# Performance work log

Measured on AMD Instinct MI355X. Metric: run time of the kernel, lower is better.

## Reference

```python
import jax, jax.numpy as jnp
import numpy as np

E_REF = 2.0e11
I_REF = 1.0e-6
Q_REF = 1.0e3
L = 1.0
N = 262144
H = 64


def setup_inputs() -> dict:
    key = jax.random.key(0)
    ks = jax.random.split(key, 8)
    x = jax.random.uniform(ks[0], (N, 1), dtype=jnp.float32) * L
    E = (0.5 + jax.random.uniform(ks[1], (N, 1), dtype=jnp.float32)) * E_REF
    I = (0.5 + jax.random.uniform(ks[2], (N, 1), dtype=jnp.float32)) * I_REF
    q = (0.5 + jax.random.uniform(ks[3], (N, 1), dtype=jnp.float32)) * Q_REF

    def xavier(k, fin, fout):
        std = np.sqrt(2.0 / (fin + fout)).astype(np.float32)
        return jax.random.normal(k, (fin, fout), dtype=jnp.float32) * std

    return dict(
        x=x, E=E, I=I, q=q,
        W1=xavier(ks[4], 4, H), b1=jnp.zeros((H,), jnp.float32),
        W2=xavier(ks[5], H, H), b2=jnp.zeros((H,), jnp.float32),
        W3=xavier(ks[6], H, H), b3=jnp.zeros((H,), jnp.float32),
        W4=xavier(ks[7], H, 1), b4=jnp.zeros((1,), jnp.float32),
    )


def reference(x, E, I, q, W1, b1, W2, b2, W3, b3, W4, b4):
    # per-point scalar network psi(x; E, I, q)
    def psi_scalar(xs, feats):  # xs: scalar, feats: [3] = (E/E_ref, I/I_ref, q/q_ref)
        inp = jnp.concatenate([xs[None], feats])  # [4]
        h = jnp.tanh(inp @ W1 + b1)
        h = jnp.tanh(h @ W2 + b2)
        h = jnp.tanh(h @ W3 + b3)
        return (h @ W4 + b4)[0]

    d1 = jax.grad(psi_scalar)
    d2 = jax.grad(d1)
    d3 = jax.grad(d2)
    d4 = jax.grad(d3)

    feats = jnp.concatenate([E / E_REF, I / I_REF, q / Q_REF], axis=1)  # [N,3]
    xs = x[:, 0]  # [N]

    psi   = jax.vmap(psi_scalar)(xs, feats)[:, None]
    px    = jax.vmap(d1)(xs, feats)[:, None]
    pxx   = jax.vmap(d2)(xs, feats)[:, None]
    pxxx  = jax.vmap(d3)(xs, feats)[:, None]
    pxxxx = jax.vmap(d4)(xs, feats)[:, None]

    x2 = x * x
    w      = x2 * psi
    w_x    = 2 * x * psi + x2 * px
    w_xx   = 2 * psi + 4 * x * px + x2 * pxx
    w_xxx  = 6 * px + 6 * x * pxx + x2 * pxxx
    w_xxxx = 12 * pxx + 8 * x * pxxx + x2 * pxxxx

    eps = jnp.finfo(x.dtype).eps
    s = q * L ** 4 / (E * I + eps)
    # stacked outputs: [5, N, 1] = (w, w_x, w_xx, w_xxx, w_xxxx)
    return jnp.stack([
        s * w,
        s * (w_x / L),
        s * (w_xx / L ** 2),
        s * (w_xxx / L ** 3),
        s * (w_xxxx / L ** 4),
    ])
```

## Files before the change

### kernel.cpp

```cpp
#include <hip/hip_runtime.h>
#include <stdint.h>

typedef _Float16 f16x2 __attribute__((ext_vector_type(2)));
typedef _Float16 f16x4 __attribute__((ext_vector_type(4)));
typedef _Float16 f16x8 __attribute__((ext_vector_type(8)));
typedef __fp16   hf16x2 __attribute__((ext_vector_type(2)));
typedef float    f32x4 __attribute__((ext_vector_type(4)));
typedef uint4    u128a __attribute__((may_alias));

union HU   { uint32_t u; _Float16 h[2]; };
union B128 { uint4 q; f16x8 v; };
union PK2  { hf16x2 a; f16x2 b; };

__device__ __forceinline__ f16x2 pkrtz2(float lo, float hi) {
  PK2 u; u.a = __builtin_amdgcn_cvt_pkrtz(lo, hi);
  return u.b;
}

__device__ __forceinline__ f16x8 cat4(f16x2 a, f16x2 b, f16x2 c, f16x2 d) {
  f16x4 ab = __builtin_shufflevector(a, b, 0, 1, 2, 3);
  f16x4 cd = __builtin_shufflevector(c, d, 0, 1, 2, 3);
  return __builtin_shufflevector(ab, cd, 0, 1, 2, 3, 4, 5, 6, 7);
}

__device__ __forceinline__ float fast_exp2(float x) {
#if __has_builtin(__builtin_amdgcn_exp2f)
  return __builtin_amdgcn_exp2f(x);
#else
  return exp2f(x);
#endif
}
__device__ __forceinline__ float fast_rcp(float x) {
#if __has_builtin(__builtin_amdgcn_rcpf)
  return __builtin_amdgcn_rcpf(x);
#else
  return 1.0f / x;
#endif
}

__device__ __forceinline__ void tanh_jets(float u0, float u1, float u2, float u3, float u4,
                                          float& t0, float& t1, float& t2, float& t3, float& t4) {
  float aa = fminf(fmaf(2.8853900817779268f, u0, 2.0f), 127.0f);
  float e4 = fast_exp2(aa);
  float r  = fast_rcp(fmaf(0.25f, e4, 1.0f));
  t0 = fmaf(-2.0f, r, 1.0f);
  float v0 = e4 * (r * r);
  t1 = v0 * u1;
  float h1 = t0 * t1;
  t2 = fmaf(u2, v0, -(u1 * h1));
  float v2 = -fmaf(t0 + t0, t2, t1 * t1);
  t3 = fmaf(u3, v0, fmaf(-1.3333333333f * u2, h1, 0.3333333333f * u1 * v2));
  float v3 = -2.0f * fmaf(t0, t3, t1 * t2);
  t4 = fmaf(u4, v0, fmaf(-1.5f * u3, h1, fmaf(0.5f * u2, v2, 0.25f * u1 * v3)));
}

__device__ __forceinline__ void tanh_jets1(float u0, float u1,
                                           float& t0, float& t1, float& t2, float& t3, float& t4) {
  float aa = fminf(fmaf(2.8853900817779268f, u0, 2.0f), 127.0f);
  float e4 = fast_exp2(aa);
  float r  = fast_rcp(fmaf(0.25f, e4, 1.0f));
  t0 = fmaf(-2.0f, r, 1.0f);
  float v0 = e4 * (r * r);
  t1 = v0 * u1;
  float h1 = t0 * t1;
  t2 = -(u1 * h1);
  float v2 = -fmaf(t0 + t0, t2, t1 * t1);
  t3 = 0.3333333333f * (u1 * v2);
  float v3 = -2.0f * fmaf(t0, t3, t1 * t2);
  t4 = 0.25f * (u1 * v3);
}

__global__ void prep_kernel(const float* __restrict__ W1, const float* __restrict__ b1,
                            const float* __restrict__ W2, const float* __restrict__ W3,
                            const float* __restrict__ W4, uint32_t* __restrict__ ws) {
  const int t = threadIdx.x;
  float* P1 = (float*)ws;
  if (t < 64) {
    P1[t * 8 + 0] = W1[0 * 64 + t];
    P1[t * 8 + 1] = W1[1 * 64 + t];
    P1[t * 8 + 2] = W1[2 * 64 + t];
    P1[t * 8 + 3] = W1[3 * 64 + t];
    P1[t * 8 + 4] = b1[t];
    P1[t * 8 + 5] = 0.f; P1[t * 8 + 6] = 0.f; P1[t * 8 + 7] = 0.f;
  }
  for (int idx = t; idx < 2048; idx += 256) {
    const int fi = idx >> 8;
    const int tm = fi >> 1, s = fi & 1;
    const int l  = (idx >> 2) & 63;
    const int pj = idx & 3;
    const int g  = l >> 4;
    const int mm = 16 * tm + (l & 15);
    const int j0 = 2 * pj, j1 = 2 * pj + 1;
    const int k2a = 16 * g + 8 * s + j0;
    const int k2b = 16 * g + 8 * s + j1;
    HU a; a.h[0] = (_Float16)W2[k2a * 64 + mm]; a.h[1] = (_Float16)W2[k2b * 64 + mm];
    ws[512 + idx] = a.u;
    const int k3a = 32 * s + 16 * (j0 >> 2) + 4 * g + (j0 & 3);
    const int k3b = 32 * s + 16 * (j1 >> 2) + 4 * g + (j1 & 3);
    HU b; b.h[0] = (_Float16)W3[k3a * 64 + mm]; b.h[1] = (_Float16)W3[k3b * 64 + mm];
    ws[2560 + idx] = b.u;
  }
  if (t < 64) {
    ws[4608 + t] = __float_as_uint(W4[t]);
  }
}

#define MFMA16(A, B, C) __builtin_amdgcn_mfma_f32_16x16x32_f16((A), (B), (C), 0, 0, 0)

#define MM5H(AF, T, S, BF) { \
    acc[0][T] = MFMA16((AF).v, BF[0][S], acc[0][T]); \
    acc[1][T] = MFMA16((AF).v, BF[1][S], acc[1][T]); \
    acc[2][T] = MFMA16((AF).v, BF[2][S], acc[2][T]); \
    acc[3][T] = MFMA16((AF).v, BF[3][S], acc[3][T]); \
    acc[4][T] = MFMA16((AF).v, BF[4][S], acc[4][T]); }

#define INIT2(BIAS, HH) { \
  const float4 bv0_ = *(const float4*)((BIAS) + 16 * (2 * (HH) + 0) + 4 * g); \
  const float4 bv1_ = *(const float4*)((BIAS) + 16 * (2 * (HH) + 1) + 4 * g); \
  acc[0][0] = (f32x4){bv0_.x, bv0_.y, bv0_.z, bv0_.w}; \
  acc[0][1] = (f32x4){bv1_.x, bv1_.y, bv1_.z, bv1_.w}; \
  acc[1][0] = (f32x4){0.f, 0.f, 0.f, 0.f}; acc[1][1] = (f32x4){0.f, 0.f, 0.f, 0.f}; \
  acc[2][0] = (f32x4){0.f, 0.f, 0.f, 0.f}; acc[2][1] = (f32x4){0.f, 0.f, 0.f, 0.f}; \
  acc[3][0] = (f32x4){0.f, 0.f, 0.f, 0.f}; acc[3][1] = (f32x4){0.f, 0.f, 0.f, 0.f}; \
  acc[4][0] = (f32x4){0.f, 0.f, 0.f, 0.f}; acc[4][1] = (f32x4){0.f, 0.f, 0.f, 0.f}; }

#define L1P(S, DI, D0, D1, D2, D3, D4) { \
  const int h0_ = 16 * g + 8 * (S) + 2 * (DI); \
  float A0_, A1_, A2_, A3_, A4_, B0_, B1_, B2_, B3_, B4_; \
  { const float4 wv_ = *(const float4*)(P1f + h0_ * 8); \
    const float bb_  = P1f[h0_ * 8 + 4]; \
    float u0_ = fmaf(wv_.x, x, fmaf(wv_.y, f1, fmaf(wv_.z, f2, fmaf(wv_.w, f3, bb_)))); \
    tanh_jets1(u0_, wv_.x, A0_, A1_, A2_, A3_, A4_); } \
  { const float4 wv_ = *(const float4*)(P1f + (h0_ + 1) * 8); \
    const float bb_  = P1f[(h0_ + 1) * 8 + 4]; \
    float u0_ = fmaf(wv_.x, x, fmaf(wv_.y, f1, fmaf(wv_.z, f2, fmaf(wv_.w, f3, bb_)))); \
    tanh_jets1(u0_, wv_.x, B0_, B1_, B2_, B3_, B4_); } \
  D0 = pkrtz2(A0_, B0_); D1 = pkrtz2(A1_, B1_); D2 = pkrtz2(A2_, B2_); \
  D3 = pkrtz2(A3_, B3_); D4 = pkrtz2(A4_, B4_); }

#define L1HALF(S) { \
  f16x2 qa0, qa1, qa2, qa3, qa4, qb0, qb1, qb2, qb3, qb4; \
  f16x2 qc0, qc1, qc2, qc3, qc4, qd0, qd1, qd2, qd3, qd4; \
  L1P(S, 0, qa0, qa1, qa2, qa3, qa4) \
  L1P(S, 1, qb0, qb1, qb2, qb3, qb4) \
  L1P(S, 2, qc0, qc1, qc2, qc3, qc4) \
  L1P(S, 3, qd0, qd1, qd2, qd3, qd4) \
  bf2[0][S] = cat4(qa0, qb0, qc0, qd0); \
  bf2[1][S] = cat4(qa1, qb1, qc1, qd1); \
  bf2[2][S] = cat4(qa2, qb2, qc2, qd2); \
  bf2[3][S] = cat4(qa3, qb3, qc3, qd3); \
  bf2[4][S] = cat4(qa4, qb4, qc4, qd4); }

#define PKTILE2(T, E0, E1, E2, E3, E4, F0, F1, F2, F3, F4) { \
  float A0_, A1_, A2_, A3_, A4_, B0_, B1_, B2_, B3_, B4_; \
  tanh_jets(acc[0][T][0], acc[1][T][0], acc[2][T][0], acc[3][T][0], acc[4][T][0], \
            A0_, A1_, A2_, A3_, A4_); \
  tanh_jets(acc[0][T][1], acc[1][T][1], acc[2][T][1], acc[3][T][1], acc[4][T][1], \
            B0_, B1_, B2_, B3_, B4_); \
  E0 = pkrtz2(A0_, B0_); E1 = pkrtz2(A1_, B1_); E2 = pkrtz2(A2_, B2_); \
  E3 = pkrtz2(A3_, B3_); E4 = pkrtz2(A4_, B4_); \
  tanh_jets(acc[0][T][2], acc[1][T][2], acc[2][T][2], acc[3][T][2], acc[4][T][2], \
            A0_, A1_, A2_, A3_, A4_); \
  tanh_jets(acc[0][T][3], acc[1][T][3], acc[2][T][3], acc[3][T][3], acc[4][T][3], \
            B0_, B1_, B2_, B3_, B4_); \
  F0 = pkrtz2(A0_, B0_); F1 = pkrtz2(A1_, B1_); F2 = pkrtz2(A2_, B2_); \
  F3 = pkrtz2(A3_, B3_); F4 = pkrtz2(A4_, B4_); }

#define PKHALF2(HH) { \
  f16x2 ve0, ve1, ve2, ve3, ve4, vf0, vf1, vf2, vf3, vf4; \
  f16x2 vm0, vm1, vm2, vm3, vm4, vn0, vn1, vn2, vn3, vn4; \
  PKTILE2(0, ve0, ve1, ve2, ve3, ve4, vf0, vf1, vf2, vf3, vf4) \
  PKTILE2(1, vm0, vm1, vm2, vm3, vm4, vn0, vn1, vn2, vn3, vn4) \
  bf3[0][HH] = cat4(ve0, vf0, vm0, vn0); \
  bf3[1][HH] = cat4(ve1, vf1, vm1, vn1); \
  bf3[2][HH] = cat4(ve2, vf2, vm2, vn2); \
  bf3[3][HH] = cat4(ve3, vf3, vm3, vn3); \
  bf3[4][HH] = cat4(ve4, vf4, vm4, vn4); }

#define L3T(T, TMG) { \
  const float4 wv4_ = *(const float4*)(W4f + 16 * (TMG) + 4 * g); \
  float t0_, t1_, t2_, t3_, t4_; \
  tanh_jets(acc[0][T][0], acc[1][T][0], acc[2][T][0], acc[3][T][0], acc[4][T][0], \
            t0_, t1_, t2_, t3_, t4_); \
  zz[0] = fmaf(wv4_.x, t0_, zz[0]); zz[1] = fmaf(wv4_.x, t1_, zz[1]); \
  zz[2] = fmaf(wv4_.x, t2_, zz[2]); zz[3] = fmaf(wv4_.x, t3_, zz[3]); \
  zz[4] = fmaf(wv4_.x, t4_, zz[4]); \
  tanh_jets(acc[0][T][1], acc[1][T][1], acc[2][T][1], acc[3][T][1], acc[4][T][1], \
            t0_, t1_, t2_, t3_, t4_); \
  zz[0] = fmaf(wv4_.y, t0_, zz[0]); zz[1] = fmaf(wv4_.y, t1_, zz[1]); \
  zz[2] = fmaf(wv4_.y, t2_, zz[2]); zz[3] = fmaf(wv4_.y, t3_, zz[3]); \
  zz[4] = fmaf(wv4_.y, t4_, zz[4]); \
  tanh_jets(acc[0][T][2], acc[1][T][2], acc[2][T][2], acc[3][T][2], acc[4][T][2], \
            t0_, t1_, t2_, t3_, t4_); \
  zz[0] = fmaf(wv4_.z, t0_, zz[0]); zz[1] = fmaf(wv4_.z, t1_, zz[1]); \
  zz[2] = fmaf(wv4_.z, t2_, zz[2]); zz[3] = fmaf(wv4_.z, t3_, zz[3]); \
  zz[4] = fmaf(wv4_.z, t4_, zz[4]); \
  tanh_jets(acc[0][T][3], acc[1][T][3], acc[2][T][3], acc[3][T][3], acc[4][T][3], \
            t0_, t1_, t2_, t3_, t4_); \
  zz[0] = fmaf(wv4_.w, t0_, zz[0]); zz[1] = fmaf(wv4_.w, t1_, zz[1]); \
  zz[2] = fmaf(wv4_.w, t2_, zz[2]); zz[3] = fmaf(wv4_.w, t3_, zz[3]); \
  zz[4] = fmaf(wv4_.w, t4_, zz[4]); }

__global__ __launch_bounds__(64, 4)
void beam_kernel(const float* __restrict__ X, const float* __restrict__ Ein,
                 const float* __restrict__ Iin, const float* __restrict__ Qin,
                 const float* __restrict__ b2, const float* __restrict__ b3,
                 const float* __restrict__ b4, const uint32_t* __restrict__ ws,
                 float* __restrict__ out, int n) {
  const int l   = threadIdx.x & 63;
  const int g   = l >> 4;
  const int p   = l & 15;
  int i = blockIdx.x * 16 + p;
  if (i >= n) i = n - 1;

  const float x  = X[i];
  const float Ev = Ein[i], Iv = Iin[i], qv = Qin[i];
  const float f1 = Ev * 5.0e-12f;
  const float f2 = Iv * 1.0e6f;
  const float f3 = qv * 1.0e-3f;
  const float sf = qv * fast_rcp(fmaf(Ev, Iv, 1.1920929e-7f));

  const float* P1f = (const float*)ws;
  const float* W4f = (const float*)(ws + 4608);

  f16x8 bf2[5][2];
  L1HALF(0)
  L1HALF(1)

  f16x8 bf3[5][2];
  f32x4 acc[5][2];
  {
    B128 Fa, Fb, Fc, Fd;
    Fa.q = *(const u128a*)(ws + 512 + ((0) * 64 + l) * 4);
    Fb.q = *(const u128a*)(ws + 512 + ((1) * 64 + l) * 4);
    Fc.q = *(const u128a*)(ws + 512 + ((2) * 64 + l) * 4);
    Fd.q = *(const u128a*)(ws + 512 + ((3) * 64 + l) * 4);
    INIT2(b2, 0)
    MM5H(Fa, 0, 0, bf2) MM5H(Fc, 1, 0, bf2)
    MM5H(Fb, 0, 1, bf2) MM5H(Fd, 1, 1, bf2)
    PKHALF2(0)
  }
  {
    B128 Fa, Fb, Fc, Fd;
    Fa.q = *(const u128a*)(ws + 512 + ((4) * 64 + l) * 4);
    Fb.q = *(const u128a*)(ws + 512 + ((5) * 64 + l) * 4);
    Fc.q = *(const u128a*)(ws + 512 + ((6) * 64 + l) * 4);
    Fd.q = *(const u128a*)(ws + 512 + ((7) * 64 + l) * 4);
    INIT2(b2, 1)
    MM5H(Fa, 0, 0, bf2) MM5H(Fc, 1, 0, bf2)
    MM5H(Fb, 0, 1, bf2) MM5H(Fd, 1, 1, bf2)
    PKHALF2(1)
  }

  float zz[5] = {0.f, 0.f, 0.f, 0.f, 0.f};
  {
    B128 Fa, Fb, Fc, Fd;
    Fa.q = *(const u128a*)(ws + 2560 + ((0) * 64 + l) * 4);
    Fb.q = *(const u128a*)(ws + 2560 + ((1) * 64 + l) * 4);
    Fc.q = *(const u128a*)(ws + 2560 + ((2) * 64 + l) * 4);
    Fd.q = *(const u128a*)(ws + 2560 + ((3) * 64 + l) * 4);
    INIT2(b3, 0)
    MM5H(Fa, 0, 0, bf3) MM5H(Fc, 1, 0, bf3)
    MM5H(Fb, 0, 1, bf3) MM5H(Fd, 1, 1, bf3)
    L3T(0, 0)
    L3T(1, 1)
  }
  {
    B128 Fa, Fb, Fc, Fd;
    Fa.q = *(const u128a*)(ws + 2560 + ((4) * 64 + l) * 4);
    Fb.q = *(const u128a*)(ws + 2560 + ((5) * 64 + l) * 4);
    Fc.q = *(const u128a*)(ws + 2560 + ((6) * 64 + l) * 4);
    Fd.q = *(const u128a*)(ws + 2560 + ((7) * 64 + l) * 4);
    INIT2(b3, 1)
    MM5H(Fa, 0, 0, bf3) MM5H(Fc, 1, 0, bf3)
    MM5H(Fb, 0, 1, bf3) MM5H(Fd, 1, 1, bf3)
    L3T(0, 2)
    L3T(1, 3)
  }

  #pragma unroll
  for (int k = 0; k < 5; ++k) {
    zz[k] += __shfl_xor(zz[k], 16, 64);
    zz[k] += __shfl_xor(zz[k], 32, 64);
  }

  const float psi   = zz[0] + b4[0];
  const float px    = zz[1];
  const float pxx   = 2.0f  * zz[2];
  const float pxxx  = 6.0f  * zz[3];
  const float pxxxx = 24.0f * zz[4];
  const float x2 = x * x;
  const float o0 = sf * (x2 * psi);
  const float o1 = sf * fmaf(2.0f * x, psi, x2 * px);
  const float o2 = sf * (fmaf(4.0f * x, px, 2.0f * psi) + x2 * pxx);
  const float o3 = sf * (fmaf(6.0f * x, pxx, 6.0f * px) + x2 * pxxx);
  const float o4 = sf * (fmaf(8.0f * x, pxxx, 12.0f * pxx) + x2 * pxxxx);
  const float og = (g == 0) ? o0 : (g == 1) ? o1 : (g == 2) ? o2 : o3;
  out[g * n + i] = og;
  if (l < 16) out[4 * n + i] = o4;
}

extern "C" void kernel_launch(void* const* d_in, const int* in_sizes, int n_in,
                              void* d_out, int out_size, void* d_ws, size_t ws_size,
                              hipStream_t stream) {
  const float* X  = (const float*)d_in[0];
  const float* E  = (const float*)d_in[1];
  const float* I  = (const float*)d_in[2];
  const float* q  = (const float*)d_in[3];
  const float* W1 = (const float*)d_in[4];
  const float* b1 = (const float*)d_in[5];
  const float* W2 = (const float*)d_in[6];
  const float* b2 = (const float*)d_in[7];
  const float* W3 = (const float*)d_in[8];
  const float* b3 = (const float*)d_in[9];
  const float* W4 = (const float*)d_in[10];
  const float* b4 = (const float*)d_in[11];
  const int n = in_sizes[0];
  uint32_t* ws = (uint32_t*)d_ws;
  float* out = (float*)d_out;

  prep_kernel<<<dim3(1), dim3(256), 0, stream>>>(W1, b1, W2, W3, W4, ws);
  beam_kernel<<<dim3((n + 15) / 16), dim3(64), 0, stream>>>(X, E, I, q, b2, b3, b4, ws, out, n);
}
```

Measured before the change: 59.82 us.

## Compute tanh derivative jets in packed fp16 and use fdot2 for output layer

```diff
diff --git a/kernel.cpp b/kernel.cpp
--- a/kernel.cpp
+++ b/kernel.cpp
@@ -9,18 +9,31 @@
 typedef uint4    u128a __attribute__((may_alias));
 
 union HU   { uint32_t u; _Float16 h[2]; };
+union HF2  { uint32_t u; f16x2 v; };
 union B128 { uint4 q; f16x8 v; };
 union PK2  { hf16x2 a; f16x2 b; };
 
 __device__ __forceinline__ f16x2 pkrtz2(float lo, float hi) {
   PK2 u; u.a = __builtin_amdgcn_cvt_pkrtz(lo, hi);
   return u.b;
+}
+
+__device__ __forceinline__ f16x2 spl(float c) {
+  f16x2 v; v[0] = (_Float16)c; v[1] = (_Float16)c; return v;
 }
 
 __device__ __forceinline__ f16x8 cat4(f16x2 a, f16x2 b, f16x2 c, f16x2 d) {
   f16x4 ab = __builtin_shufflevector(a, b, 0, 1, 2, 3);
   f16x4 cd = __builtin_shufflevector(c, d, 0, 1, 2, 3);
   return __builtin_shufflevector(ab, cd, 0, 1, 2, 3, 4, 5, 6, 7);
+}
+
+__device__ __forceinline__ float fdot2f(f16x2 a, f16x2 b, float c) {
+#if __has_builtin(__builtin_amdgcn_fdot2)
+  return __builtin_amdgcn_fdot2(a, b, c, false);
+#else
+  return fmaf((float)a[1], (float)b[1], fmaf((float)a[0], (float)b[0], c));
+#endif
 }
 
 __device__ __forceinline__ float fast_exp2(float x) {
@@ -38,36 +51,48 @@
 #endif
 }
 
-__device__ __forceinline__ void tanh_jets(float u0, float u1, float u2, float u3, float u4,
-                                          float& t0, float& t1, float& t2, float& t3, float& t4) {
-  float aa = fminf(fmaf(2.8853900817779268f, u0, 2.0f), 127.0f);
-  float e4 = fast_exp2(aa);
-  float r  = fast_rcp(fmaf(0.25f, e4, 1.0f));
-  t0 = fmaf(-2.0f, r, 1.0f);
-  float v0 = e4 * (r * r);
-  t1 = v0 * u1;
-  float h1 = t0 * t1;
-  t2 = fmaf(u2, v0, -(u1 * h1));
-  float v2 = -fmaf(t0 + t0, t2, t1 * t1);
-  t3 = fmaf(u3, v0, fmaf(-1.3333333333f * u2, h1, 0.3333333333f * u1 * v2));
-  float v3 = -2.0f * fmaf(t0, t3, t1 * t2);
-  t4 = fmaf(u4, v0, fmaf(-1.5f * u3, h1, fmaf(0.5f * u2, v2, 0.25f * u1 * v3)));
-}
-
-__device__ __forceinline__ void tanh_jets1(float u0, float u1,
-                                           float& t0, float& t1, float& t2, float& t3, float& t4) {
-  float aa = fminf(fmaf(2.8853900817779268f, u0, 2.0f), 127.0f);
-  float e4 = fast_exp2(aa);
-  float r  = fast_rcp(fmaf(0.25f, e4, 1.0f));
-  t0 = fmaf(-2.0f, r, 1.0f);
-  float v0 = e4 * (r * r);
-  t1 = v0 * u1;
-  float h1 = t0 * t1;
-  t2 = -(u1 * h1);
-  float v2 = -fmaf(t0 + t0, t2, t1 * t1);
-  t3 = 0.3333333333f * (u1 * v2);
-  float v3 = -2.0f * fmaf(t0, t3, t1 * t2);
-  t4 = 0.25f * (u1 * v3);
+__device__ __forceinline__ void jets_pk(
+    float z0A, float z1A, float z2A, float z3A, float z4A,
+    float z0B, float z1B, float z2B, float z3B, float z4B,
+    f16x2& T0, f16x2& T1, f16x2& T2, f16x2& T3, f16x2& T4) {
+  float aaA = fminf(fmaf(2.8853900817779268f, z0A, 2.0f), 127.0f);
+  float aaB = fminf(fmaf(2.8853900817779268f, z0B, 2.0f), 127.0f);
+  float e4A = fast_exp2(aaA), e4B = fast_exp2(aaB);
+  float rA  = fast_rcp(fmaf(0.25f, e4A, 1.0f));
+  float rB  = fast_rcp(fmaf(0.25f, e4B, 1.0f));
+  T0 = pkrtz2(fmaf(-2.0f, rA, 1.0f), fmaf(-2.0f, rB, 1.0f));
+  f16x2 V0 = pkrtz2(e4A * (rA * rA), e4B * (rB * rB));
+  f16x2 U1 = pkrtz2(z1A, z1B);
+  f16x2 U2 = pkrtz2(z2A, z2B);
+  f16x2 U3 = pkrtz2(z3A, z3B);
+  f16x2 U4 = pkrtz2(z4A, z4B);
+  T1 = V0 * U1;
+  f16x2 h1  = T0 * T1;
+  T2 = U2 * V0 - U1 * h1;
+  f16x2 v2n = (T0 + T0) * T2 + T1 * T1;
+  T3 = U3 * V0 - spl(1.3333334f) * (U2 * h1) - spl(0.33333334f) * (U1 * v2n);
+  f16x2 v3h = T0 * T3 + T1 * T2;
+  T4 = U4 * V0 - spl(1.5f) * (U3 * h1) - spl(0.5f) * (U2 * v2n) - spl(0.5f) * (U1 * v3h);
+}
+
+__device__ __forceinline__ void jets_pk1(
+    float z0A, float z1A, float z0B, float z1B,
+    f16x2& T0, f16x2& T1, f16x2& T2, f16x2& T3, f16x2& T4) {
+  float aaA = fminf(fmaf(2.8853900817779268f, z0A, 2.0f), 127.0f);
+  float aaB = fminf(fmaf(2.8853900817779268f, z0B, 2.0f), 127.0f);
+  float e4A = fast_exp2(aaA), e4B = fast_exp2(aaB);
+  float rA  = fast_rcp(fmaf(0.25f, e4A, 1.0f));
+  float rB  = fast_rcp(fmaf(0.25f, e4B, 1.0f));
+  T0 = pkrtz2(fmaf(-2.0f, rA, 1.0f), fmaf(-2.0f, rB, 1.0f));
+  f16x2 V0 = pkrtz2(e4A * (rA * rA), e4B * (rB * rB));
+  f16x2 U1 = pkrtz2(z1A, z1B);
+  T1 = V0 * U1;
+  f16x2 h1  = T0 * T1;
+  T2 = -(U1 * h1);
+  f16x2 v2n = (T0 + T0) * T2 + T1 * T1;
+  T3 = -spl(0.33333334f) * (U1 * v2n);
+  f16x2 v3h = T0 * T3 + T1 * T2;
+  T4 = -spl(0.5f) * (U1 * v3h);
 }
 
 __global__ void prep_kernel(const float* __restrict__ W1, const float* __restrict__ b1,
@@ -100,8 +125,13 @@
     HU b; b.h[0] = (_Float16)W3[k3a * 64 + mm]; b.h[1] = (_Float16)W3[k3b * 64 + mm];
     ws[2560 + idx] = b.u;
   }
-  if (t < 64) {
-    ws[4608 + t] = __float_as_uint(W4[t]);
+  for (int t2 = t; t2 < 512; t2 += 256) {
+    const int lq = t2 >> 3;
+    const int tm = (t2 >> 1) & 3;
+    const int hf = t2 & 1;
+    const int h0 = 16 * tm + 4 * (lq >> 4) + 2 * hf;
+    HU a; a.h[0] = (_Float16)W4[h0]; a.h[1] = (_Float16)W4[h0 + 1];
+    ws[4608 + t2] = a.u;
   }
 }
 
@@ -126,17 +156,13 @@
 
 #define L1P(S, DI, D0, D1, D2, D3, D4) { \
   const int h0_ = 16 * g + 8 * (S) + 2 * (DI); \
-  float A0_, A1_, A2_, A3_, A4_, B0_, B1_, B2_, B3_, B4_; \
-  { const float4 wv_ = *(const float4*)(P1f + h0_ * 8); \
-    const float bb_  = P1f[h0_ * 8 + 4]; \
-    float u0_ = fmaf(wv_.x, x, fmaf(wv_.y, f1, fmaf(wv_.z, f2, fmaf(wv_.w, f3, bb_)))); \
-    tanh_jets1(u0_, wv_.x, A0_, A1_, A2_, A3_, A4_); } \
-  { const float4 wv_ = *(const float4*)(P1f + (h0_ + 1) * 8); \
-    const float bb_  = P1f[(h0_ + 1) * 8 + 4]; \
-    float u0_ = fmaf(wv_.x, x, fmaf(wv_.y, f1, fmaf(wv_.z, f2, fmaf(wv_.w, f3, bb_)))); \
-    tanh_jets1(u0_, wv_.x, B0_, B1_, B2_, B3_, B4_); } \
-  D0 = pkrtz2(A0_, B0_); D1 = pkrtz2(A1_, B1_); D2 = pkrtz2(A2_, B2_); \
-  D3 = pkrtz2(A3_, B3_); D4 = pkrtz2(A4_, B4_); }
+  const float4 wvA_ = *(const float4*)(P1f + h0_ * 8); \
+  const float bbA_  = P1f[h0_ * 8 + 4]; \
+  const float u0A_  = fmaf(wvA_.x, x, fmaf(wvA_.y, f1, fmaf(wvA_.z, f2, fmaf(wvA_.w, f3, bbA_)))); \
+  const float4 wvB_ = *(const float4*)(P1f + (h0_ + 1) * 8); \
+  const float bbB_  = P1f[(h0_ + 1) * 8 + 4]; \
+  const float u0B_  = fmaf(wvB_.x, x, fmaf(wvB_.y, f1, fmaf(wvB_.z, f2, fmaf(wvB_.w, f3, bbB_)))); \
+  jets_pk1(u0A_, wvA_.x, u0B_, wvB_.x, D0, D1, D2, D3, D4); }
 
 #define L1HALF(S) { \
   f16x2 qa0, qa1, qa2, qa3, qa4, qb0, qb1, qb2, qb3, qb4; \
@@ -152,19 +178,12 @@
   bf2[4][S] = cat4(qa4, qb4, qc4, qd4); }
 
 #define PKTILE2(T, E0, E1, E2, E3, E4, F0, F1, F2, F3, F4) { \
-  float A0_, A1_, A2_, A3_, A4_, B0_, B1_, B2_, B3_, B4_; \
-  tanh_jets(acc[0][T][0], acc[1][T][0], acc[2][T][0], acc[3][T][0], acc[4][T][0], \
-            A0_, A1_, A2_, A3_, A4_); \
-  tanh_jets(acc[0][T][1], acc[1][T][1], acc[2][T][1], acc[3][T][1], acc[4][T][1], \
-            B0_, B1_, B2_, B3_, B4_); \
-  E0 = pkrtz2(A0_, B0_); E1 = pkrtz2(A1_, B1_); E2 = pkrtz2(A2_, B2_); \
-  E3 = pkrtz2(A3_, B3_); E4 = pkrtz2(A4_, B4_); \
-  tanh_jets(acc[0][T][2], acc[1][T][2], acc[2][T][2], acc[3][T][2], acc[4][T][2], \
-            A0_, A1_, A2_, A3_, A4_); \
-  tanh_jets(acc[0][T][3], acc[1][T][3], acc[2][T][3], acc[3][T][3], acc[4][T][3], \
-            B0_, B1_, B2_, B3_, B4_); \
-  F0 = pkrtz2(A0_, B0_); F1 = pkrtz2(A1_, B1_); F2 = pkrtz2(A2_, B2_); \
-  F3 = pkrtz2(A3_, B3_); F4 = pkrtz2(A4_, B4_); }
+  jets_pk(acc[0][T][0], acc[1][T][0], acc[2][T][0], acc[3][T][0], acc[4][T][0], \
+          acc[0][T][1], acc[1][T][1], acc[2][T][1], acc[3][T][1], acc[4][T][1], \
+          E0, E1, E2, E3, E4); \
+  jets_pk(acc[0][T][2], acc[1][T][2], acc[2][T][2], acc[3][T][2], acc[4][T][2], \
+          acc[0][T][3], acc[1][T][3], acc[2][T][3], acc[3][T][3], acc[4][T][3], \
+          F0, F1, F2, F3, F4); }
 
 #define PKHALF2(HH) { \
   f16x2 ve0, ve1, ve2, ve3, ve4, vf0, vf1, vf2, vf3, vf4; \
@@ -178,28 +197,22 @@
   bf3[4][HH] = cat4(ve4, vf4, vm4, vn4); }
 
 #define L3T(T, TMG) { \
-  const float4 wv4_ = *(const float4*)(W4f + 16 * (TMG) + 4 * g); \
-  float t0_, t1_, t2_, t3_, t4_; \
-  tanh_jets(acc[0][T][0], acc[1][T][0], acc[2][T][0], acc[3][T][0], acc[4][T][0], \
-            t0_, t1_, t2_, t3_, t4_); \
-  zz[0] = fmaf(wv4_.x, t0_, zz[0]); zz[1] = fmaf(wv4_.x, t1_, zz[1]); \
-  zz[2] = fmaf(wv4_.x, t2_, zz[2]); zz[3] = fmaf(wv4_.x, t3_, zz[3]); \
-  zz[4] = fmaf(wv4_.x, t4_, zz[4]); \
-  tanh_jets(acc[0][T][1], acc[1][T][1], acc[2][T][1], acc[3][T][1], acc[4][T][1], \
-            t0_, t1_, t2_, t3_, t4_); \
-  zz[0] = fmaf(wv4_.y, t0_, zz[0]); zz[1] = fmaf(wv4_.y, t1_, zz[1]); \
-  zz[2] = fmaf(wv4_.y, t2_, zz[2]); zz[3] = fmaf(wv4_.y, t3_, zz[3]); \
-  zz[4] = fmaf(wv4_.y, t4_, zz[4]); \
-  tanh_jets(acc[0][T][2], acc[1][T][2], acc[2][T][2], acc[3][T][2], acc[4][T][2], \
-            t0_, t1_, t2_, t3_, t4_); \
-  zz[0] = fmaf(wv4_.z, t0_, zz[0]); zz[1] = fmaf(wv4_.z, t1_, zz[1]); \
-  zz[2] = fmaf(wv4_.z, t2_, zz[2]); zz[3] = fmaf(wv4_.z, t3_, zz[3]); \
-  zz[4] = fmaf(wv4_.z, t4_, zz[4]); \
-  tanh_jets(acc[0][T][3], acc[1][T][3], acc[2][T][3], acc[3][T][3], acc[4][T][3], \
-            t0_, t1_, t2_, t3_, t4_); \
-  zz[0] = fmaf(wv4_.w, t0_, zz[0]); zz[1] = fmaf(wv4_.w, t1_, zz[1]); \
-  zz[2] = fmaf(wv4_.w, t2_, zz[2]); zz[3] = fmaf(wv4_.w, t3_, zz[3]); \
-  zz[4] = fmaf(wv4_.w, t4_, zz[4]); }
+  HF2 wa_, wb_; \
+  wa_.u = W4p[l * 8 + (TMG) * 2 + 0]; \
+  wb_.u = W4p[l * 8 + (TMG) * 2 + 1]; \
+  f16x2 t0_, t1_, t2_, t3_, t4_; \
+  jets_pk(acc[0][T][0], acc[1][T][0], acc[2][T][0], acc[3][T][0], acc[4][T][0], \
+          acc[0][T][1], acc[1][T][1], acc[2][T][1], acc[3][T][1], acc[4][T][1], \
+          t0_, t1_, t2_, t3_, t4_); \
+  zz[0] = fdot2f(t0_, wa_.v, zz[0]); zz[1] = fdot2f(t1_, wa_.v, zz[1]); \
+  zz[2] = fdot2f(t2_, wa_.v, zz[2]); zz[3] = fdot2f(t3_, wa_.v, zz[3]); \
+  zz[4] = fdot2f(t4_, wa_.v, zz[4]); \
+  jets_pk(acc[0][T][2], acc[1][T][2], acc[2][T][2], acc[3][T][2], acc[4][T][2], \
+          acc[0][T][3], acc[1][T][3], acc[2][T][3], acc[3][T][3], acc[4][T][3], \
+          t0_, t1_, t2_, t3_, t4_); \
+  zz[0] = fdot2f(t0_, wb_.v, zz[0]); zz[1] = fdot2f(t1_, wb_.v, zz[1]); \
+  zz[2] = fdot2f(t2_, wb_.v, zz[2]); zz[3] = fdot2f(t3_, wb_.v, zz[3]); \
+  zz[4] = fdot2f(t4_, wb_.v, zz[4]); }
 
 __global__ __launch_bounds__(64, 4)
 void beam_kernel(const float* __restrict__ X, const float* __restrict__ Ein,
@@ -220,8 +233,8 @@
   const float f3 = qv * 1.0e-3f;
   const float sf = qv * fast_rcp(fmaf(Ev, Iv, 1.1920929e-7f));
 
-  const float* P1f = (const float*)ws;
-  const float* W4f = (const float*)(ws + 4608);
+  const float*    P1f = (const float*)ws;
+  const uint32_t* W4p = ws + 4608;
 
   f16x8 bf2[5][2];
   L1HALF(0)
```

Result: faster. 53.44 us, median of 2 (-10.7%).
